# Kernel optimization log

Hardware: AMD Instinct MI355X
Metric: run time of the kernel (lower is better)

## Reference

```python
import jax, jax.numpy as jnp
import numpy as np


def setup_inputs() -> dict:
    key = jax.random.key(0)
    k1, k2 = jax.random.split(key)
    node_num = 10000
    n_edges = 640000
    d = 128
    embs = jax.random.normal(k1, (node_num, d), dtype=jnp.float32)
    ratings = jax.random.randint(k2, (n_edges, 2), 0, node_num, dtype=jnp.int32)
    return {"embs": embs, "ratings": ratings, "node_num": node_num}


def reference(embs, ratings, node_num):
    # edge endpoints: row (source) and column (neighbor) indices
    r0 = ratings[:, 0]
    r1 = ratings[:, 1]
    # edge dot-product attention scores  [E]
    scores = jnp.sum(embs[r0] * embs[r1], axis=-1)
    # sparse row-wise softmax (torch.sparse.softmax over dim=1)
    seg_max = jax.ops.segment_max(scores, r0, num_segments=node_num)
    seg_max = jnp.where(jnp.isfinite(seg_max), seg_max, jnp.float32(0.0))  # empty rows
    ex = jnp.exp(scores - seg_max[r0])
    denom = jax.ops.segment_sum(ex, r0, num_segments=node_num)
    attn = ex / denom[r0]
    # attention weights are detached in the original module
    attn = jax.lax.stop_gradient(attn)
    # sparse mm aggregation: out[i] = sum_{e: r0[e]=i} attn[e] * embs[r1[e]]
    out = jax.ops.segment_sum(attn[:, None] * embs[r1], r0, num_segments=node_num)
    return out
```

## Files before the change

kernel.cpp:

```cpp
#include <hip/hip_runtime.h>
#include <hip/hip_bf16.h>
#include <hip/hip_fp16.h>
#include <math.h>


#define K_CHUNKS 256
#define NODE_LDS 10240
#define NPAD 10240
#define STAGE_LDS 2560
#define EXP_CLAMP 80.0f
#define MAXE_N 256

using half2v = _Float16 __attribute__((ext_vector_type(2)));

__device__ __forceinline__ half2v u2h(unsigned int x) {
    return __builtin_bit_cast(half2v, x);
}

__global__ __launch_bounds__(1024) void build_kernel(const int2* __restrict__ ratings,
                             unsigned short* __restrict__ mtmp,
                             unsigned short* __restrict__ staging,
                             int n_edges, int node_num, int chunk_size) {
    __shared__ int hist[NODE_LDS];
    __shared__ unsigned short stage[STAGE_LDS];
    __shared__ int lds_ws[16];
    __shared__ int lds_wp[16];

    int tid  = threadIdx.x;
    int lane = tid & 63;
    int wid  = tid >> 6;
    int k    = blockIdx.x;

    for (int i = tid; i < NODE_LDS; i += 1024) hist[i] = 0;
    __syncthreads();

    int base = k * chunk_size;
    int end  = base + chunk_size; if (end > n_edges) end = n_edges;

    int e0i = base + tid, e1i = e0i + 1024, e2i = e1i + 1024;
    bool h0 = e0i < end, h1 = e1i < end, h2 = e2i < end;
    int2 r0v = h0 ? ratings[e0i] : make_int2(0, 0);
    int2 r1v = h1 ? ratings[e1i] : make_int2(0, 0);
    int2 r2v = h2 ? ratings[e2i] : make_int2(0, 0);

    if (h0) atomicAdd(&hist[r0v.x], 1);
    if (h1) atomicAdd(&hist[r1v.x], 1);
    if (h2) atomicAdd(&hist[r2v.x], 1);
    for (int e = base + 3072 + tid; e < end; e += 1024)
        atomicAdd(&hist[ratings[e].x], 1);
    __syncthreads();

    const int B = NODE_LDS / 1024;
    int b0 = tid * B;
    int c[B];
    int local = 0;
    #pragma unroll
    for (int j = 0; j < B; ++j) {
        c[j] = hist[b0 + j];
        local += c[j];
    }
    int incl = local;
    #pragma unroll
    for (int off = 1; off < 64; off <<= 1) {
        int t = __shfl_up(incl, off, 64);
        if (lane >= off) incl += t;
    }
    if (lane == 63) lds_ws[wid] = incl;
    __syncthreads();
    if (wid == 0 && lane < 16) {
        int wv = lds_ws[lane];
        #pragma unroll
        for (int off = 1; off < 16; off <<= 1) {
            int t = __shfl_up(wv, off, 64);
            if (lane >= off) wv += t;
        }
        lds_wp[lane] = wv;
    }
    __syncthreads();
    int run = ((wid > 0) ? lds_wp[wid - 1] : 0) + (incl - local);

    unsigned int mpack[B / 2];
    #pragma unroll
    for (int j = 0; j < B; ++j) {
        int i = b0 + j;
        int cc = (c[j] > 15) ? 15 : c[j];
        unsigned int m = (((unsigned int)run << 4) | (unsigned int)cc) & 0xffffu;
        if (j & 1) mpack[j >> 1] |= m << 16;
        else       mpack[j >> 1]  = m;
        hist[i] = run;
        run += c[j];
    }
    {
        unsigned int* mrow2 = (unsigned int*)(mtmp + (size_t)k * NPAD) + tid * (B / 2);
        #pragma unroll
        for (int jj = 0; jj < B / 2; ++jj) mrow2[jj] = mpack[jj];
    }
    __syncthreads();

    if (h0) { int p = atomicAdd(&hist[r0v.x], 1); if (p < STAGE_LDS) stage[p] = (unsigned short)r0v.y; }
    if (h1) { int p = atomicAdd(&hist[r1v.x], 1); if (p < STAGE_LDS) stage[p] = (unsigned short)r1v.y; }
    if (h2) { int p = atomicAdd(&hist[r2v.x], 1); if (p < STAGE_LDS) stage[p] = (unsigned short)r2v.y; }
    for (int e = base + 3072 + tid; e < end; e += 1024) {
        int2 r = ratings[e];
        int p = atomicAdd(&hist[r.x], 1);
        if (p < STAGE_LDS) stage[p] = (unsigned short)r.y;
    }
    __syncthreads();

    int nsh = end - base;
    unsigned int* g  = (unsigned int*)(staging + (size_t)k * chunk_size);
    unsigned int* sg = (unsigned int*)stage;
    int nu = (nsh + 1) >> 1;
    for (int i = tid; i < nu; i += 1024) g[i] = sg[i];
}

__global__ __launch_bounds__(256) void transpose_kernel(const unsigned short* __restrict__ mtmp,
                                                        unsigned short* __restrict__ meta_t,
                                                        const float4* __restrict__ embs4,
                                                        ushort4* __restrict__ embs16,
                                                        int node_num) {
    __shared__ unsigned short tile[64][66];
    int n0 = blockIdx.x * 64;
    int k0 = blockIdx.y * 64;
    int tx = threadIdx.x & 63;
    int ty = threadIdx.x >> 6;
    #pragma unroll
    for (int r = 0; r < 64; r += 4) {
        int n = n0 + tx;
        tile[r + ty][tx] = (n < node_num) ? mtmp[(size_t)(k0 + r + ty) * NPAD + n] : 0;
    }
    __syncthreads();
    #pragma unroll
    for (int r = 0; r < 64; r += 4) {
        int n = n0 + r + ty;
        if (n < node_num)
            meta_t[(size_t)n * K_CHUNKS + k0 + tx] = tile[tx][r + ty];
    }

    int nblocks = gridDim.x * gridDim.y;
    int bid = blockIdx.y * gridDim.x + blockIdx.x;
    int nf4 = node_num * 32;
    int per = (nf4 + nblocks - 1) / nblocks;
    int s0 = bid * per;
    int s1 = s0 + per; if (s1 > nf4) s1 = nf4;
    for (int i = s0 + (int)threadIdx.x; i < s1; i += 256) {
        float4 v = embs4[i];
        __half hx = __float2half(v.x), hy = __float2half(v.y);
        __half hz = __float2half(v.z), hw = __float2half(v.w);
        ushort4 o;
        o.x = *reinterpret_cast<unsigned short*>(&hx);
        o.y = *reinterpret_cast<unsigned short*>(&hy);
        o.z = *reinterpret_cast<unsigned short*>(&hz);
        o.w = *reinterpret_cast<unsigned short*>(&hw);
        embs16[i] = o;
    }
}

__global__ __launch_bounds__(256) void node_kernel(
                            const unsigned short* __restrict__ embs16,
                            const unsigned short* __restrict__ meta_t,
                            const unsigned short* __restrict__ staging,
                            float* __restrict__ out,
                            int node_num, int chunk_size) {
    __shared__ int s_r1[4][MAXE_N];

    int tid   = threadIdx.x;
    int lane  = tid & 63;
    int wid   = tid >> 6;
    int g     = lane >> 4;
    int t     = lane & 15;
    int n     = blockIdx.x * 4 + wid;
    bool nvalid = (n < node_num);
    int nc    = nvalid ? n : 0;

    const uint2* mrow = (const uint2*)(meta_t + (size_t)nc * K_CHUNKS);
    uint2 mm = mrow[lane];
    unsigned int f[4];
    f[0] = mm.x & 0xffffu; f[1] = mm.x >> 16;
    f[2] = mm.y & 0xffffu; f[3] = mm.y >> 16;
    int c[4], o[4];
    #pragma unroll
    for (int j = 0; j < 4; ++j) {
        c[j] = nvalid ? (int)(f[j] & 15u) : 0;
        o[j] = (int)(f[j] >> 4);
    }
    int cnt = (c[0] + c[1]) + (c[2] + c[3]);
    int incl = cnt;
    #pragma unroll
    for (int off = 1; off < 64; off <<= 1) {
        int tt = __shfl_up(incl, off, 64);
        if (lane >= off) incl += tt;
    }
    int basep = incl - cnt;
    int E = __shfl(incl, 63, 64);
    if (E > MAXE_N) E = MAXE_N;

    unsigned short sv0[4], sv1[4];
    #pragma unroll
    for (int j = 0; j < 4; ++j) {
        const unsigned short* sp = staging + (size_t)(4 * lane + j) * chunk_size + o[j];
        sv0[j] = sp[0];
        sv1[j] = sp[1];
    }
    {
        int idx = basep;
        #pragma unroll
        for (int j = 0; j < 4; ++j) {
            if (c[j] > 0) {
                if (idx < MAXE_N) s_r1[wid][idx] = (int)sv0[j];
                ++idx;
                if (c[j] > 1) {
                    if (idx < MAXE_N) s_r1[wid][idx] = (int)sv1[j];
                    ++idx;
                    if (c[j] > 2) {
                        const unsigned short* sp = staging + (size_t)(4 * lane + j) * chunk_size + o[j];
                        for (int q = 2; q < c[j]; ++q) {
                            if (idx < MAXE_N) s_r1[wid][idx] = (int)sp[q];
                            ++idx;
                        }
                    }
                }
            }
        }
    }

    uint4 au = ((const uint4*)(embs16 + (size_t)nc * 128))[t];

    float l = 0.f;
    float acc[8];
    #pragma unroll
    for (int j = 0; j < 8; ++j) acc[j] = 0.f;

    bool vc[4]; uint4 uc[4];
    #pragma unroll
    for (int b = 0; b < 4; ++b) {
        int ix = b * 4 + g;
        vc[b] = ix < E;
        int r1 = vc[b] ? s_r1[wid][ix] : 0;
        uc[b] = ((const uint4*)(embs16 + (size_t)r1 * 128))[t];
    }

    for (int base = 0; base < E; base += 16) {
        bool vn[4]; uint4 un[4];
        #pragma unroll
        for (int b = 0; b < 4; ++b) {
            int ix = base + 16 + b * 4 + g;
            vn[b] = ix < E;
            int r1 = vn[b] ? s_r1[wid][ix] : 0;
            un[b] = ((const uint4*)(embs16 + (size_t)r1 * 128))[t];
        }

        float s[4];
        #pragma unroll
        for (int b = 0; b < 4; ++b) {
            float d = __builtin_amdgcn_fdot2(u2h(uc[b].x), u2h(au.x), 0.f, false);
            d = __builtin_amdgcn_fdot2(u2h(uc[b].y), u2h(au.y), d, false);
            d = __builtin_amdgcn_fdot2(u2h(uc[b].z), u2h(au.z), d, false);
            d = __builtin_amdgcn_fdot2(u2h(uc[b].w), u2h(au.w), d, false);
            s[b] = d;
        }
        #pragma unroll
        for (int b = 0; b < 4; ++b) {
            #pragma unroll
            for (int off = 1; off < 16; off <<= 1)
                s[b] += __shfl_xor(s[b], off, 64);
        }
        float p[4];
        #pragma unroll
        for (int b = 0; b < 4; ++b)
            p[b] = vc[b] ? __expf(fminf(s[b], EXP_CLAMP)) : 0.f;
        l += (p[0] + p[1]) + (p[2] + p[3]);

        #pragma unroll
        for (int b = 0; b < 4; ++b) {
            half2v h0 = u2h(uc[b].x), h1 = u2h(uc[b].y);
            half2v h2 = u2h(uc[b].z), h3 = u2h(uc[b].w);
            acc[0] = fmaf(p[b], (float)h0[0], acc[0]);
            acc[1] = fmaf(p[b], (float)h0[1], acc[1]);
            acc[2] = fmaf(p[b], (float)h1[0], acc[2]);
            acc[3] = fmaf(p[b], (float)h1[1], acc[3]);
            acc[4] = fmaf(p[b], (float)h2[0], acc[4]);
            acc[5] = fmaf(p[b], (float)h2[1], acc[5]);
            acc[6] = fmaf(p[b], (float)h3[0], acc[6]);
            acc[7] = fmaf(p[b], (float)h3[1], acc[7]);
        }

        #pragma unroll
        for (int b = 0; b < 4; ++b) { uc[b] = un[b]; vc[b] = vn[b]; }
    }

    #pragma unroll
    for (int off = 16; off <= 32; off <<= 1) {
        l += __shfl_xor(l, off, 64);
        #pragma unroll
        for (int j = 0; j < 8; ++j) acc[j] += __shfl_xor(acc[j], off, 64);
    }

    if (g == 0 && nvalid) {
        float inv = (l > 0.f) ? 1.f / l : 0.f;
        float4* orow = (float4*)(out + (size_t)n * 128);
        orow[2 * t]     = make_float4(acc[0] * inv, acc[1] * inv, acc[2] * inv, acc[3] * inv);
        orow[2 * t + 1] = make_float4(acc[4] * inv, acc[5] * inv, acc[6] * inv, acc[7] * inv);
    }
}

extern "C" void kernel_launch(void* const* d_in, const int* in_sizes, int n_in,
                              void* d_out, int out_size, void* d_ws, size_t ws_size,
                              hipStream_t stream) {
    const float* embs    = (const float*)d_in[0];
    const int*   ratings = (const int*)d_in[1];
    const int d        = 128;
    const int node_num = in_sizes[0] / d;
    const int n_edges  = in_sizes[1] / 2;
    float* out = (float*)d_out;

    int chunk_size = (n_edges + K_CHUNKS - 1) / K_CHUNKS;
    if (chunk_size & 1) chunk_size += 1;

    auto align256 = [](size_t x) { return (x + 255) & ~(size_t)255; };
    char* ws = (char*)d_ws;
    unsigned short* mtmp = (unsigned short*)ws;
    ws += align256((size_t)K_CHUNKS * NPAD * 2);
    unsigned short* meta_t = (unsigned short*)ws;
    ws += align256((size_t)node_num * K_CHUNKS * 2);
    unsigned short* staging = (unsigned short*)ws;
    ws += align256((size_t)K_CHUNKS * chunk_size * 2);
    unsigned short* embs16 = (unsigned short*)ws;
    ws += align256((size_t)node_num * 128 * 2);

    build_kernel<<<K_CHUNKS, 1024, 0, stream>>>(
        (const int2*)ratings, mtmp, staging, n_edges, node_num, chunk_size);

    {
        dim3 grid((node_num + 63) / 64, K_CHUNKS / 64);
        transpose_kernel<<<grid, 256, 0, stream>>>(
            mtmp, meta_t, (const float4*)embs, (ushort4*)embs16, node_num);
    }

    {
        int blocks = (node_num + 3) / 4;
        node_kernel<<<blocks, 256, 0, stream>>>(
            embs16, meta_t, staging, out, node_num, chunk_size);
    }
}
```

Baseline: 95.53 us.

## Move fp16 conversion into build kernel and widen staging reads in node kernel

The fp32-to-fp16 embedding conversion moves from the transpose kernel into the build kernel, where it can overlap with the ratings loads and histogram atomics, leaving the transpose kernel lighter. The node kernel now fetches each chunk's neighbor indices with one aligned 16-byte load instead of separate 2-byte loads, pulling out the first two entries from registers. The load of the node's own embedding is also issued earlier to hide its latency. The staging buffer gets 32 bytes of padding so the wide aligned reads stay in bounds, and the build kernel takes on more per-block work.

```diff
diff --git a/kernel.cpp b/kernel.cpp
--- a/kernel.cpp
+++ b/kernel.cpp
@@ -17,9 +17,17 @@
     return __builtin_bit_cast(half2v, x);
 }
 
+__device__ __forceinline__ unsigned short ext8(unsigned long long lo,
+                                               unsigned long long hi, int q) {
+    unsigned long long v = (q & 4) ? hi : lo;
+    return (unsigned short)(v >> ((q & 3) * 16));
+}
+
 __global__ __launch_bounds__(1024) void build_kernel(const int2* __restrict__ ratings,
                              unsigned short* __restrict__ mtmp,
                              unsigned short* __restrict__ staging,
+                             const float4* __restrict__ embs4,
+                             ushort4* __restrict__ embs16,
                              int n_edges, int node_num, int chunk_size) {
     __shared__ int hist[NODE_LDS];
     __shared__ unsigned short stage[STAGE_LDS];
@@ -42,6 +50,24 @@
     int2 r0v = h0 ? ratings[e0i] : make_int2(0, 0);
     int2 r1v = h1 ? ratings[e1i] : make_int2(0, 0);
     int2 r2v = h2 ? ratings[e2i] : make_int2(0, 0);
+
+    {
+        int nf4 = node_num * 32;
+        int per = (nf4 + (int)gridDim.x - 1) / (int)gridDim.x;
+        int s0 = k * per;
+        int s1 = s0 + per; if (s1 > nf4) s1 = nf4;
+        for (int i = s0 + tid; i < s1; i += 1024) {
+            float4 v = embs4[i];
+            __half hx = __float2half(v.x), hy = __float2half(v.y);
+            __half hz = __float2half(v.z), hw = __float2half(v.w);
+            ushort4 o;
+            o.x = *reinterpret_cast<unsigned short*>(&hx);
+            o.y = *reinterpret_cast<unsigned short*>(&hy);
+            o.z = *reinterpret_cast<unsigned short*>(&hz);
+            o.w = *reinterpret_cast<unsigned short*>(&hw);
+            embs16[i] = o;
+        }
+    }
 
     if (h0) atomicAdd(&hist[r0v.x], 1);
     if (h1) atomicAdd(&hist[r1v.x], 1);
@@ -116,8 +142,6 @@
 
 __global__ __launch_bounds__(256) void transpose_kernel(const unsigned short* __restrict__ mtmp,
                                                         unsigned short* __restrict__ meta_t,
-                                                        const float4* __restrict__ embs4,
-                                                        ushort4* __restrict__ embs16,
                                                         int node_num) {
     __shared__ unsigned short tile[64][66];
     int n0 = blockIdx.x * 64;
@@ -135,24 +159,6 @@
         int n = n0 + r + ty;
         if (n < node_num)
             meta_t[(size_t)n * K_CHUNKS + k0 + tx] = tile[tx][r + ty];
-    }
-
-    int nblocks = gridDim.x * gridDim.y;
-    int bid = blockIdx.y * gridDim.x + blockIdx.x;
-    int nf4 = node_num * 32;
-    int per = (nf4 + nblocks - 1) / nblocks;
-    int s0 = bid * per;
-    int s1 = s0 + per; if (s1 > nf4) s1 = nf4;
-    for (int i = s0 + (int)threadIdx.x; i < s1; i += 256) {
-        float4 v = embs4[i];
-        __half hx = __float2half(v.x), hy = __float2half(v.y);
-        __half hz = __float2half(v.z), hw = __float2half(v.w);
-        ushort4 o;
-        o.x = *reinterpret_cast<unsigned short*>(&hx);
-        o.y = *reinterpret_cast<unsigned short*>(&hy);
-        o.z = *reinterpret_cast<unsigned short*>(&hz);
-        o.w = *reinterpret_cast<unsigned short*>(&hw);
-        embs16[i] = o;
     }
 }
 
@@ -175,6 +181,8 @@
 
     const uint2* mrow = (const uint2*)(meta_t + (size_t)nc * K_CHUNKS);
     uint2 mm = mrow[lane];
+    uint4 au = ((const uint4*)(embs16 + (size_t)nc * 128))[t];
+
     unsigned int f[4];
     f[0] = mm.x & 0xffffu; f[1] = mm.x >> 16;
     f[2] = mm.y & 0xffffu; f[3] = mm.y >> 16;
@@ -195,26 +203,41 @@
     int E = __shfl(incl, 63, 64);
     if (E > MAXE_N) E = MAXE_N;
 
-    unsigned short sv0[4], sv1[4];
+    unsigned long long wlo[4], whi[4];
+    size_t Lb[4];
+    int sh[4];
     #pragma unroll
     for (int j = 0; j < 4; ++j) {
-        const unsigned short* sp = staging + (size_t)(4 * lane + j) * chunk_size + o[j];
-        sv0[j] = sp[0];
-        sv1[j] = sp[1];
+        Lb[j] = (size_t)(4 * lane + j) * chunk_size + o[j];
+        sh[j] = (int)(Lb[j] & 7);
+        wlo[j] = 0; whi[j] = 0;
+        if (c[j] > 0) {
+            uint4 w = *(const uint4*)(staging + (Lb[j] & ~(size_t)7));
+            wlo[j] = ((unsigned long long)w.y << 32) | w.x;
+            whi[j] = ((unsigned long long)w.w << 32) | w.z;
+        }
     }
     {
         int idx = basep;
         #pragma unroll
         for (int j = 0; j < 4; ++j) {
             if (c[j] > 0) {
-                if (idx < MAXE_N) s_r1[wid][idx] = (int)sv0[j];
+                if (idx < MAXE_N) s_r1[wid][idx] = (int)ext8(wlo[j], whi[j], sh[j]);
                 ++idx;
                 if (c[j] > 1) {
-                    if (idx < MAXE_N) s_r1[wid][idx] = (int)sv1[j];
-                    ++idx;
-                    if (c[j] > 2) {
-                        const unsigned short* sp = staging + (size_t)(4 * lane + j) * chunk_size + o[j];
-                        for (int q = 2; q < c[j]; ++q) {
+                    if (sh[j] < 7) {
+                        if (idx < MAXE_N) s_r1[wid][idx] = (int)ext8(wlo[j], whi[j], sh[j] + 1);
+                        ++idx;
+                        if (c[j] > 2) {
+                            const unsigned short* sp = staging + Lb[j];
+                            for (int q = 2; q < c[j]; ++q) {
+                                if (idx < MAXE_N) s_r1[wid][idx] = (int)sp[q];
+                                ++idx;
+                            }
+                        }
+                    } else {
+                        const unsigned short* sp = staging + Lb[j];
+                        for (int q = 1; q < c[j]; ++q) {
                             if (idx < MAXE_N) s_r1[wid][idx] = (int)sp[q];
                             ++idx;
                         }
@@ -223,8 +246,6 @@
             }
         }
     }
-
-    uint4 au = ((const uint4*)(embs16 + (size_t)nc * 128))[t];
 
     float l = 0.f;
     float acc[8];
@@ -324,17 +345,17 @@
     unsigned short* meta_t = (unsigned short*)ws;
     ws += align256((size_t)node_num * K_CHUNKS * 2);
     unsigned short* staging = (unsigned short*)ws;
-    ws += align256((size_t)K_CHUNKS * chunk_size * 2);
+    ws += align256((size_t)K_CHUNKS * chunk_size * 2 + 32);
     unsigned short* embs16 = (unsigned short*)ws;
     ws += align256((size_t)node_num * 128 * 2);
 
     build_kernel<<<K_CHUNKS, 1024, 0, stream>>>(
-        (const int2*)ratings, mtmp, staging, n_edges, node_num, chunk_size);
+        (const int2*)ratings, mtmp, staging,
+        (const float4*)embs, (ushort4*)embs16, n_edges, node_num, chunk_size);
 
     {
         dim3 grid((node_num + 63) / 64, K_CHUNKS / 64);
-        transpose_kernel<<<grid, 256, 0, stream>>>(
-            mtmp, meta_t, (const float4*)embs, (ushort4*)embs16, node_num);
+        transpose_kernel<<<grid, 256, 0, stream>>>(mtmp, meta_t, node_num);
     }
 
     {
```

Result: no change. 93.83 us (-1.8%).

## Drop transpose kernel, fuse fp16 conversion into build, read metadata strided

Applied to the files above, without the earlier changes.

Removes the separate transpose kernel. The fp32-to-fp16 embedding conversion moves into the build kernel, and node_kernel reads per-chunk metadata straight from the untransposed mtmp array with strided 2-byte loads. This saves one launch and a full metadata round trip through memory, at the cost of uncoalesced metadata reads in node_kernel. The neighbor-embedding prefetch is also reduced from full register rows to indices only, with a launch_bounds occupancy hint of 8, trading load latency hiding for fewer registers.

```diff
diff --git a/kernel.cpp b/kernel.cpp
--- a/kernel.cpp
+++ b/kernel.cpp
@@ -20,6 +20,8 @@
 __global__ __launch_bounds__(1024) void build_kernel(const int2* __restrict__ ratings,
                              unsigned short* __restrict__ mtmp,
                              unsigned short* __restrict__ staging,
+                             const float4* __restrict__ embs4,
+                             ushort4* __restrict__ embs16,
                              int n_edges, int node_num, int chunk_size) {
     __shared__ int hist[NODE_LDS];
     __shared__ unsigned short stage[STAGE_LDS];
@@ -42,6 +44,24 @@
     int2 r0v = h0 ? ratings[e0i] : make_int2(0, 0);
     int2 r1v = h1 ? ratings[e1i] : make_int2(0, 0);
     int2 r2v = h2 ? ratings[e2i] : make_int2(0, 0);
+
+    {
+        int nf4 = node_num * 32;
+        int per = (nf4 + (int)gridDim.x - 1) / (int)gridDim.x;
+        int s0 = k * per;
+        int s1 = s0 + per; if (s1 > nf4) s1 = nf4;
+        for (int i = s0 + tid; i < s1; i += 1024) {
+            float4 v = embs4[i];
+            __half hx = __float2half(v.x), hy = __float2half(v.y);
+            __half hz = __float2half(v.z), hw = __float2half(v.w);
+            ushort4 o;
+            o.x = *reinterpret_cast<unsigned short*>(&hx);
+            o.y = *reinterpret_cast<unsigned short*>(&hy);
+            o.z = *reinterpret_cast<unsigned short*>(&hz);
+            o.w = *reinterpret_cast<unsigned short*>(&hw);
+            embs16[i] = o;
+        }
+    }
 
     if (h0) atomicAdd(&hist[r0v.x], 1);
     if (h1) atomicAdd(&hist[r1v.x], 1);
@@ -114,51 +134,9 @@
     for (int i = tid; i < nu; i += 1024) g[i] = sg[i];
 }
 
-__global__ __launch_bounds__(256) void transpose_kernel(const unsigned short* __restrict__ mtmp,
-                                                        unsigned short* __restrict__ meta_t,
-                                                        const float4* __restrict__ embs4,
-                                                        ushort4* __restrict__ embs16,
-                                                        int node_num) {
-    __shared__ unsigned short tile[64][66];
-    int n0 = blockIdx.x * 64;
-    int k0 = blockIdx.y * 64;
-    int tx = threadIdx.x & 63;
-    int ty = threadIdx.x >> 6;
-    #pragma unroll
-    for (int r = 0; r < 64; r += 4) {
-        int n = n0 + tx;
-        tile[r + ty][tx] = (n < node_num) ? mtmp[(size_t)(k0 + r + ty) * NPAD + n] : 0;
-    }
-    __syncthreads();
-    #pragma unroll
-    for (int r = 0; r < 64; r += 4) {
-        int n = n0 + r + ty;
-        if (n < node_num)
-            meta_t[(size_t)n * K_CHUNKS + k0 + tx] = tile[tx][r + ty];
-    }
-
-    int nblocks = gridDim.x * gridDim.y;
-    int bid = blockIdx.y * gridDim.x + blockIdx.x;
-    int nf4 = node_num * 32;
-    int per = (nf4 + nblocks - 1) / nblocks;
-    int s0 = bid * per;
-    int s1 = s0 + per; if (s1 > nf4) s1 = nf4;
-    for (int i = s0 + (int)threadIdx.x; i < s1; i += 256) {
-        float4 v = embs4[i];
-        __half hx = __float2half(v.x), hy = __float2half(v.y);
-        __half hz = __float2half(v.z), hw = __float2half(v.w);
-        ushort4 o;
-        o.x = *reinterpret_cast<unsigned short*>(&hx);
-        o.y = *reinterpret_cast<unsigned short*>(&hy);
-        o.z = *reinterpret_cast<unsigned short*>(&hz);
-        o.w = *reinterpret_cast<unsigned short*>(&hw);
-        embs16[i] = o;
-    }
-}
-
-__global__ __launch_bounds__(256) void node_kernel(
+__global__ __launch_bounds__(256, 8) void node_kernel(
                             const unsigned short* __restrict__ embs16,
-                            const unsigned short* __restrict__ meta_t,
+                            const unsigned short* __restrict__ mtmp,
                             const unsigned short* __restrict__ staging,
                             float* __restrict__ out,
                             int node_num, int chunk_size) {
@@ -173,11 +151,12 @@
     bool nvalid = (n < node_num);
     int nc    = nvalid ? n : 0;
 
-    const uint2* mrow = (const uint2*)(meta_t + (size_t)nc * K_CHUNKS);
-    uint2 mm = mrow[lane];
+    uint4 au = ((const uint4*)(embs16 + (size_t)nc * 128))[t];
+
     unsigned int f[4];
-    f[0] = mm.x & 0xffffu; f[1] = mm.x >> 16;
-    f[2] = mm.y & 0xffffu; f[3] = mm.y >> 16;
+    #pragma unroll
+    for (int j = 0; j < 4; ++j)
+        f[j] = mtmp[(size_t)(4 * lane + j) * NPAD + nc];
     int c[4], o[4];
     #pragma unroll
     for (int j = 0; j < 4; ++j) {
@@ -195,59 +174,44 @@
     int E = __shfl(incl, 63, 64);
     if (E > MAXE_N) E = MAXE_N;
 
-    unsigned short sv0[4], sv1[4];
-    #pragma unroll
-    for (int j = 0; j < 4; ++j) {
-        const unsigned short* sp = staging + (size_t)(4 * lane + j) * chunk_size + o[j];
-        sv0[j] = sp[0];
-        sv1[j] = sp[1];
-    }
     {
         int idx = basep;
         #pragma unroll
         for (int j = 0; j < 4; ++j) {
             if (c[j] > 0) {
-                if (idx < MAXE_N) s_r1[wid][idx] = (int)sv0[j];
-                ++idx;
-                if (c[j] > 1) {
-                    if (idx < MAXE_N) s_r1[wid][idx] = (int)sv1[j];
+                const unsigned short* sp =
+                    staging + (size_t)(4 * lane + j) * chunk_size + o[j];
+                for (int q = 0; q < c[j]; ++q) {
+                    if (idx < MAXE_N) s_r1[wid][idx] = (int)sp[q];
                     ++idx;
-                    if (c[j] > 2) {
-                        const unsigned short* sp = staging + (size_t)(4 * lane + j) * chunk_size + o[j];
-                        for (int q = 2; q < c[j]; ++q) {
-                            if (idx < MAXE_N) s_r1[wid][idx] = (int)sp[q];
-                            ++idx;
-                        }
-                    }
                 }
             }
         }
     }
 
-    uint4 au = ((const uint4*)(embs16 + (size_t)nc * 128))[t];
-
     float l = 0.f;
     float acc[8];
     #pragma unroll
     for (int j = 0; j < 8; ++j) acc[j] = 0.f;
 
-    bool vc[4]; uint4 uc[4];
+    int r1c[4];
     #pragma unroll
     for (int b = 0; b < 4; ++b) {
         int ix = b * 4 + g;
-        vc[b] = ix < E;
-        int r1 = vc[b] ? s_r1[wid][ix] : 0;
-        uc[b] = ((const uint4*)(embs16 + (size_t)r1 * 128))[t];
+        r1c[b] = (ix < E) ? s_r1[wid][ix] : 0;
     }
 
     for (int base = 0; base < E; base += 16) {
-        bool vn[4]; uint4 un[4];
+        uint4 uc[4];
+        #pragma unroll
+        for (int b = 0; b < 4; ++b)
+            uc[b] = ((const uint4*)(embs16 + (size_t)r1c[b] * 128))[t];
+
+        int r1n[4];
         #pragma unroll
         for (int b = 0; b < 4; ++b) {
             int ix = base + 16 + b * 4 + g;
-            vn[b] = ix < E;
-            int r1 = vn[b] ? s_r1[wid][ix] : 0;
-            un[b] = ((const uint4*)(embs16 + (size_t)r1 * 128))[t];
+            r1n[b] = (ix < E) ? s_r1[wid][ix] : 0;
         }
 
         float s[4];
@@ -268,7 +232,7 @@
         float p[4];
         #pragma unroll
         for (int b = 0; b < 4; ++b)
-            p[b] = vc[b] ? __expf(fminf(s[b], EXP_CLAMP)) : 0.f;
+            p[b] = ((base + b * 4 + g) < E) ? __expf(fminf(s[b], EXP_CLAMP)) : 0.f;
         l += (p[0] + p[1]) + (p[2] + p[3]);
 
         #pragma unroll
@@ -286,7 +250,7 @@
         }
 
         #pragma unroll
-        for (int b = 0; b < 4; ++b) { uc[b] = un[b]; vc[b] = vn[b]; }
+        for (int b = 0; b < 4; ++b) r1c[b] = r1n[b];
     }
 
     #pragma unroll
@@ -321,25 +285,18 @@
     char* ws = (char*)d_ws;
     unsigned short* mtmp = (unsigned short*)ws;
     ws += align256((size_t)K_CHUNKS * NPAD * 2);
-    unsigned short* meta_t = (unsigned short*)ws;
-    ws += align256((size_t)node_num * K_CHUNKS * 2);
     unsigned short* staging = (unsigned short*)ws;
-    ws += align256((size_t)K_CHUNKS * chunk_size * 2);
+    ws += align256((size_t)K_CHUNKS * chunk_size * 2 + 32);
     unsigned short* embs16 = (unsigned short*)ws;
     ws += align256((size_t)node_num * 128 * 2);
 
     build_kernel<<<K_CHUNKS, 1024, 0, stream>>>(
-        (const int2*)ratings, mtmp, staging, n_edges, node_num, chunk_size);
-
-    {
-        dim3 grid((node_num + 63) / 64, K_CHUNKS / 64);
-        transpose_kernel<<<grid, 256, 0, stream>>>(
-            mtmp, meta_t, (const float4*)embs, (ushort4*)embs16, node_num);
-    }
+        (const int2*)ratings, mtmp, staging,
+        (const float4*)embs, (ushort4*)embs16, n_edges, node_num, chunk_size);
 
     {
         int blocks = (node_num + 3) / 4;
         node_kernel<<<blocks, 256, 0, stream>>>(
-            embs16, meta_t, staging, out, node_num, chunk_size);
+            embs16, mtmp, staging, out, node_num, chunk_size);
     }
 }
```

After: 114.8 us. +20.1%, slower.
